# Kernel optimization log

Hardware: AMD Instinct MI355X
Metric: run time of the kernel (lower is better)

The kernel has to match this reference:

```python
import jax, jax.numpy as jnp
import numpy as np

EPS = 1e-6  # torch_npu npu_add_rms_norm default epsilon


def add_rms_norm(x1, x2, weight):
    # returns (normalized, x1+x2), matching npu_add_rms_norm's (y, rstd, x)
    x = x1 + x2
    inv = jax.lax.rsqrt(jnp.mean(x * x, axis=-1, keepdims=True) + EPS)
    return x * inv * weight, x


def dynamic_quant(y, smooth_scales=None):
    # per-row symmetric int8 dynamic quantization with optional smooth scales
    s = y * smooth_scales if smooth_scales is not None else y
    scale = jnp.max(jnp.abs(s), axis=-1) / 127.0  # [rows...]
    q = jnp.round(s / scale[..., None]).astype(jnp.int8)
    return q, scale


def setup_inputs() -> dict:
    key = jax.random.key(0)
    k1, k2, k3, k4 = jax.random.split(key, 4)
    B, S, H = 2, 4096, 4096
    x1 = jax.random.normal(k1, (B, S, H), dtype=jnp.float32)
    x2 = jax.random.normal(k2, (B, S, H), dtype=jnp.float32)
    weight = jax.random.uniform(k3, (H,), dtype=jnp.float32)
    smooth_scales = jax.random.uniform(k4, (H,), dtype=jnp.float32)
    return {"x1": x1, "x2": x2, "weight": weight, "smooth_scales": smooth_scales}


def reference(x1, x2, weight, smooth_scales):
    # block 1: add+rmsnorm then per-channel-smoothed dynamic int8 quant
    y, xOut = add_rms_norm(x1, x2, weight)
    yOut, scale1Out = dynamic_quant(y, smooth_scales)

    # block 2: same fused norm, quantize the 2D view
    y1, xOut1 = add_rms_norm(x1, x2, weight)
    h = y1.shape[-1]
    y2 = y1.reshape(-1, h)
    yOut2, scale1Out2 = dynamic_quant(y2, smooth_scales)
    y1_flat = y1.reshape(-1, h).astype(jnp.float32)

    # block 3: fused norm, quantize without smooth scales
    y3, xOut3 = add_rms_norm(x1, x2, weight)
    yOut3, scale1Out3 = dynamic_quant(y3.reshape(-1, h))
    scale1Out3_view = scale1Out3.reshape(-1, 1)

    return (yOut, xOut, scale1Out, y1_flat, xOut1, yOut2, scale1Out2,
            xOut3, yOut3, scale1Out3_view)
```

## Files before the change

kernel.cpp:

```cpp
#include <hip/hip_runtime.h>
#include <math.h>

#define HDIM 4096
#define THREADS 256
#define CHUNK 4
#define EPSV 1e-6f

typedef float f4 __attribute__((ext_vector_type(4)));

__device__ __forceinline__ float waveSum(float v) {
    #pragma unroll
    for (int o = 32; o > 0; o >>= 1) v += __shfl_xor(v, o);
    return v;
}
__device__ __forceinline__ float waveMax(float v) {
    #pragma unroll
    for (int o = 32; o > 0; o >>= 1) v = fmaxf(v, __shfl_xor(v, o));
    return v;
}

__global__ __launch_bounds__(THREADS) void fused_add_rmsnorm_quant(
    const float* __restrict__ x1, const float* __restrict__ x2,
    const float* __restrict__ w,  const float* __restrict__ sm,
    float* __restrict__ out, const long long N, const long long R)
{
    __shared__ float redS[4];
    __shared__ float redW[4];
    __shared__ float redM[4];

    const long long row  = blockIdx.x;
    const int tid  = threadIdx.x;
    const int wave = tid >> 6;
    const int lane = tid & 63;
    const long long base = row * (long long)HDIM;

    float* out_q   = out;
    float* out_x   = out + N;
    float* out_s1  = out + 2 * N;
    float* out_y   = out + 2 * N + R;
    float* out_xb  = out + 3 * N + R;
    float* out_q2  = out + 4 * N + R;
    float* out_s2  = out + 5 * N + R;
    float* out_x3  = out + 5 * N + 2 * R;
    float* out_q3  = out + 6 * N + 2 * R;
    float* out_s3  = out + 7 * N + 2 * R;

    f4 xv[CHUNK];

    float ss = 0.f, mW = 0.f, mSm = 0.f;
    #pragma unroll
    for (int c = 0; c < CHUNK; ++c) {
        const int col = c * (THREADS * 4) + tid * 4;
        const long long idx = base + col;
        const f4 a = __builtin_nontemporal_load(
            reinterpret_cast<const f4*>(x1 + idx));
        const f4 b = __builtin_nontemporal_load(
            reinterpret_cast<const f4*>(x2 + idx));
        const f4 wv  = *reinterpret_cast<const f4*>(w  + col);
        const f4 smv = *reinterpret_cast<const f4*>(sm + col);
        const f4 x = a + b;
        xv[c] = x;
        __builtin_nontemporal_store(x, reinterpret_cast<f4*>(out_x  + idx));
        __builtin_nontemporal_store(x, reinterpret_cast<f4*>(out_xb + idx));
        __builtin_nontemporal_store(x, reinterpret_cast<f4*>(out_x3 + idx));
        #pragma unroll
        for (int j = 0; j < 4; ++j) {
            const float t = x[j] * wv[j];
            ss += x[j] * x[j];
            mW  = fmaxf(mW,  fabsf(t));
            mSm = fmaxf(mSm, fabsf(t * smv[j]));
        }
    }
    ss  = waveSum(ss);
    mW  = waveMax(mW);
    mSm = waveMax(mSm);
    if (lane == 0) { redS[wave] = ss; redW[wave] = mW; redM[wave] = mSm; }
    __syncthreads();
    ss  = (redS[0] + redS[1]) + (redS[2] + redS[3]);
    mW  = fmaxf(fmaxf(redW[0], redW[1]), fmaxf(redW[2], redW[3]));
    mSm = fmaxf(fmaxf(redM[0], redM[1]), fmaxf(redM[2], redM[3]));

    const float inv    = 1.0f / sqrtf(ss * (1.0f / HDIM) + EPSV);
    const float scale1 = (inv * mSm) * (1.0f / 127.0f);
    const float scale3 = (inv * mW)  * (1.0f / 127.0f);
    const float rs1 = 1.0f / scale1;
    const float rs3 = 1.0f / scale3;

    #pragma unroll
    for (int c = 0; c < CHUNK; ++c) {
        const int col = c * (THREADS * 4) + tid * 4;
        const long long idx = base + col;
        const f4 wv  = *reinterpret_cast<const f4*>(w  + col);
        const f4 smv = *reinterpret_cast<const f4*>(sm + col);
        f4 yq, qf, q3;
        #pragma unroll
        for (int j = 0; j < 4; ++j) {
            const float x = xv[c][j];
            const float y = x * inv * wv[j];
            const float s = y * smv[j];
            yq[j] = y;
            qf[j] = rintf(s * rs1);
            q3[j] = rintf(y * rs3);
        }
        __builtin_nontemporal_store(qf, reinterpret_cast<f4*>(out_q  + idx));
        __builtin_nontemporal_store(yq, reinterpret_cast<f4*>(out_y  + idx));
        __builtin_nontemporal_store(qf, reinterpret_cast<f4*>(out_q2 + idx));
        __builtin_nontemporal_store(q3, reinterpret_cast<f4*>(out_q3 + idx));
    }
    if (tid == 0) {
        out_s1[row] = scale1;
        out_s2[row] = scale1;
        out_s3[row] = scale3;
    }
}

extern "C" void kernel_launch(void* const* d_in, const int* in_sizes, int n_in,
                              void* d_out, int out_size, void* d_ws, size_t ws_size,
                              hipStream_t stream) {
    const float* x1 = (const float*)d_in[0];
    const float* x2 = (const float*)d_in[1];
    const float* w  = (const float*)d_in[2];
    const float* sm = (const float*)d_in[3];
    float* out = (float*)d_out;

    const long long N = (long long)in_sizes[0];
    const long long R = N / HDIM;

    fused_add_rmsnorm_quant<<<dim3((unsigned)R), dim3(THREADS), 0, stream>>>(
        x1, x2, w, sm, out, N, R);
}
```

Before: 231.3 us.

## Map one wavefront per row and group stores per output stream

Each 64-lane wave now processes a whole 4096-wide row, with four rows per block, so the cross-wave LDS reduction and __syncthreads are gone. Loads are batched four at a time, and the outputs are written as separate runs per destination array, split by scheduling barriers. Each lane now holds 16 float4 values, which raises register pressure. The launch bounds ask for 4 blocks per CU, and recomputing y and q per output pass adds some ALU work.

Measured after the change: 244.6 us. 5.8% more time.

```diff
diff --git a/kernel.cpp b/kernel.cpp
--- a/kernel.cpp
+++ b/kernel.cpp
@@ -3,7 +3,7 @@
 
 #define HDIM 4096
 #define THREADS 256
-#define CHUNK 4
+#define NC 16
 #define EPSV 1e-6f
 
 typedef float f4 __attribute__((ext_vector_type(4)));
@@ -18,21 +18,21 @@
     for (int o = 32; o > 0; o >>= 1) v = fmaxf(v, __shfl_xor(v, o));
     return v;
 }
+__device__ __forceinline__ void runBreak() {
+    __builtin_amdgcn_sched_barrier(0);
+}
 
-__global__ __launch_bounds__(THREADS) void fused_add_rmsnorm_quant(
+__global__ __launch_bounds__(THREADS, 4) void fused_add_rmsnorm_quant(
     const float* __restrict__ x1, const float* __restrict__ x2,
     const float* __restrict__ w,  const float* __restrict__ sm,
     float* __restrict__ out, const long long N, const long long R)
 {
-    __shared__ float redS[4];
-    __shared__ float redW[4];
-    __shared__ float redM[4];
-
-    const long long row  = blockIdx.x;
     const int tid  = threadIdx.x;
-    const int wave = tid >> 6;
     const int lane = tid & 63;
+    const int wid  = tid >> 6;
+    const long long row  = (long long)blockIdx.x * 4 + wid;
     const long long base = row * (long long)HDIM;
+    const int colb = lane * 4;
 
     float* out_q   = out;
     float* out_x   = out + N;
@@ -45,40 +45,57 @@
     float* out_q3  = out + 6 * N + 2 * R;
     float* out_s3  = out + 7 * N + 2 * R;
 
-    f4 xv[CHUNK];
+    f4 xv[NC];
+    float ss = 0.f, mW = 0.f, mSm = 0.f;
 
-    float ss = 0.f, mW = 0.f, mSm = 0.f;
     #pragma unroll
-    for (int c = 0; c < CHUNK; ++c) {
-        const int col = c * (THREADS * 4) + tid * 4;
-        const long long idx = base + col;
-        const f4 a = __builtin_nontemporal_load(
-            reinterpret_cast<const f4*>(x1 + idx));
-        const f4 b = __builtin_nontemporal_load(
-            reinterpret_cast<const f4*>(x2 + idx));
-        const f4 wv  = *reinterpret_cast<const f4*>(w  + col);
-        const f4 smv = *reinterpret_cast<const f4*>(sm + col);
-        const f4 x = a + b;
-        xv[c] = x;
-        __builtin_nontemporal_store(x, reinterpret_cast<f4*>(out_x  + idx));
-        __builtin_nontemporal_store(x, reinterpret_cast<f4*>(out_xb + idx));
-        __builtin_nontemporal_store(x, reinterpret_cast<f4*>(out_x3 + idx));
+    for (int h = 0; h < 4; ++h) {
+        f4 a[4], b[4];
         #pragma unroll
-        for (int j = 0; j < 4; ++j) {
-            const float t = x[j] * wv[j];
-            ss += x[j] * x[j];
-            mW  = fmaxf(mW,  fabsf(t));
-            mSm = fmaxf(mSm, fabsf(t * smv[j]));
+        for (int c = 0; c < 4; ++c)
+            a[c] = __builtin_nontemporal_load(
+                reinterpret_cast<const f4*>(x1 + base + (h*4 + c)*256 + colb));
+        #pragma unroll
+        for (int c = 0; c < 4; ++c)
+            b[c] = __builtin_nontemporal_load(
+                reinterpret_cast<const f4*>(x2 + base + (h*4 + c)*256 + colb));
+        #pragma unroll
+        for (int c = 0; c < 4; ++c) {
+            const int col = (h*4 + c)*256 + colb;
+            const f4 wv  = *reinterpret_cast<const f4*>(w  + col);
+            const f4 smv = *reinterpret_cast<const f4*>(sm + col);
+            const f4 x = a[c] + b[c];
+            xv[h*4 + c] = x;
+            #pragma unroll
+            for (int j = 0; j < 4; ++j) {
+                const float t = x[j] * wv[j];
+                ss += x[j] * x[j];
+                mW  = fmaxf(mW,  fabsf(t));
+                mSm = fmaxf(mSm, fabsf(t * smv[j]));
+            }
         }
     }
+
+    runBreak();
+    #pragma unroll
+    for (int c = 0; c < NC; ++c)
+        __builtin_nontemporal_store(xv[c],
+            reinterpret_cast<f4*>(out_x  + base + c*256 + colb));
+    runBreak();
+    #pragma unroll
+    for (int c = 0; c < NC; ++c)
+        __builtin_nontemporal_store(xv[c],
+            reinterpret_cast<f4*>(out_xb + base + c*256 + colb));
+    runBreak();
+    #pragma unroll
+    for (int c = 0; c < NC; ++c)
+        __builtin_nontemporal_store(xv[c],
+            reinterpret_cast<f4*>(out_x3 + base + c*256 + colb));
+    runBreak();
+
     ss  = waveSum(ss);
     mW  = waveMax(mW);
     mSm = waveMax(mSm);
-    if (lane == 0) { redS[wave] = ss; redW[wave] = mW; redM[wave] = mSm; }
-    __syncthreads();
-    ss  = (redS[0] + redS[1]) + (redS[2] + redS[3]);
-    mW  = fmaxf(fmaxf(redW[0], redW[1]), fmaxf(redW[2], redW[3]));
-    mSm = fmaxf(fmaxf(redM[0], redM[1]), fmaxf(redM[2], redM[3]));
 
     const float inv    = 1.0f / sqrtf(ss * (1.0f / HDIM) + EPSV);
     const float scale1 = (inv * mSm) * (1.0f / 127.0f);
@@ -87,27 +104,52 @@
     const float rs3 = 1.0f / scale3;
 
     #pragma unroll
-    for (int c = 0; c < CHUNK; ++c) {
-        const int col = c * (THREADS * 4) + tid * 4;
-        const long long idx = base + col;
+    for (int c = 0; c < NC; ++c) {
+        const int col = c*256 + colb;
         const f4 wv  = *reinterpret_cast<const f4*>(w  + col);
         const f4 smv = *reinterpret_cast<const f4*>(sm + col);
-        f4 yq, qf, q3;
+        f4 qf;
         #pragma unroll
-        for (int j = 0; j < 4; ++j) {
-            const float x = xv[c][j];
-            const float y = x * inv * wv[j];
-            const float s = y * smv[j];
-            yq[j] = y;
-            qf[j] = rintf(s * rs1);
-            q3[j] = rintf(y * rs3);
-        }
-        __builtin_nontemporal_store(qf, reinterpret_cast<f4*>(out_q  + idx));
-        __builtin_nontemporal_store(yq, reinterpret_cast<f4*>(out_y  + idx));
-        __builtin_nontemporal_store(qf, reinterpret_cast<f4*>(out_q2 + idx));
-        __builtin_nontemporal_store(q3, reinterpret_cast<f4*>(out_q3 + idx));
+        for (int j = 0; j < 4; ++j)
+            qf[j] = rintf(xv[c][j] * inv * wv[j] * smv[j] * rs1);
+        __builtin_nontemporal_store(qf, reinterpret_cast<f4*>(out_q + base + col));
     }
-    if (tid == 0) {
+    runBreak();
+    #pragma unroll
+    for (int c = 0; c < NC; ++c) {
+        const int col = c*256 + colb;
+        const f4 wv = *reinterpret_cast<const f4*>(w + col);
+        f4 yq;
+        #pragma unroll
+        for (int j = 0; j < 4; ++j)
+            yq[j] = xv[c][j] * inv * wv[j];
+        __builtin_nontemporal_store(yq, reinterpret_cast<f4*>(out_y + base + col));
+    }
+    runBreak();
+    #pragma unroll
+    for (int c = 0; c < NC; ++c) {
+        const int col = c*256 + colb;
+        const f4 wv  = *reinterpret_cast<const f4*>(w  + col);
+        const f4 smv = *reinterpret_cast<const f4*>(sm + col);
+        f4 qf;
+        #pragma unroll
+        for (int j = 0; j < 4; ++j)
+            qf[j] = rintf(xv[c][j] * inv * wv[j] * smv[j] * rs1);
+        __builtin_nontemporal_store(qf, reinterpret_cast<f4*>(out_q2 + base + col));
+    }
+    runBreak();
+    #pragma unroll
+    for (int c = 0; c < NC; ++c) {
+        const int col = c*256 + colb;
+        const f4 wv = *reinterpret_cast<const f4*>(w + col);
+        f4 q3;
+        #pragma unroll
+        for (int j = 0; j < 4; ++j)
+            q3[j] = rintf(xv[c][j] * inv * wv[j] * rs3);
+        __builtin_nontemporal_store(q3, reinterpret_cast<f4*>(out_q3 + base + col));
+    }
+
+    if (lane == 0) {
         out_s1[row] = scale1;
         out_s2[row] = scale1;
         out_s3[row] = scale3;
@@ -126,6 +168,6 @@
     const long long N = (long long)in_sizes[0];
     const long long R = N / HDIM;
 
-    fused_add_rmsnorm_quant<<<dim3((unsigned)R), dim3(THREADS), 0, stream>>>(
+    fused_add_rmsnorm_quant<<<dim3((unsigned)(R / 4)), dim3(THREADS), 0, stream>>>(
         x1, x2, w, sm, out, N, R);
 }
```
